# Kernel optimization log

Hardware: AMD Instinct MI355X
Metric: run time of the kernel (lower is better)

The kernel has to match this reference:

```python
import jax, jax.numpy as jnp
from jax import lax
import numpy as np

IMG = 448          # input image H=W
FEAT = 14          # attention map H=W
STR = IMG // FEAT  # 32: feature->image stride
OUT = 112          # crop resize target
RATIOS = [(4, 4), (3, 5), (5, 3), (6, 6), (5, 7), (7, 5)]
GROUPS = [(0, 3), (3, 6)]   # ratio groups for per-group NMS
N_LIST = [4, 3]
IOU_THRESHS = [0.25, 0.25]
PROPOSALN = 7
CLASSES = 200


def _build_coords():
    coords = []
    for (rh, rw) in RATIOS:
        for r in range(FEAT - rh + 1):
            for c in range(FEAT - rw + 1):
                coords.append([r * STR, c * STR, (r + rh) * STR - 1, (c + rw) * STR - 1])
    return np.array(coords, dtype=np.float32)

COORDS = jnp.asarray(_build_coords())                      # [602, 4] image-space boxes (inclusive)
WINDOW_NUMS = [(FEAT - rh + 1) * (FEAT - rw + 1) for rh, rw in RATIOS]
GROUP_BOUNDS = []
for (s, e) in GROUPS:
    GROUP_BOUNDS.append((sum(WINDOW_NUMS[:s]), sum(WINDOW_NUMS[:e])))


def _window_scores(att):
    # att: [B,1,FEAT,FEAT] -> [B, total_windows]; AvgPool2d(ratio, stride=1) per ratio, flattened row-major
    scs = []
    for (rh, rw) in RATIOS:
        s = lax.reduce_window(att[:, 0], 0.0, lax.add, (1, rh, rw), (1, 1, 1), 'VALID') / (rh * rw)
        scs.append(s.reshape(att.shape[0], -1))
    return jnp.concatenate(scs, axis=1)


def _iou(box, boxes):
    x0 = jnp.maximum(box[0], boxes[:, 0]); y0 = jnp.maximum(box[1], boxes[:, 1])
    x1 = jnp.minimum(box[2], boxes[:, 2]); y1 = jnp.minimum(box[3], boxes[:, 3])
    inter = jnp.maximum(x1 - x0 + 1, 0.0) * jnp.maximum(y1 - y0 + 1, 0.0)
    a1 = (box[2] - box[0] + 1) * (box[3] - box[1] + 1)
    a2 = (boxes[:, 2] - boxes[:, 0] + 1) * (boxes[:, 3] - boxes[:, 1] + 1)
    return inter / (a1 + a2 - inter)


def _nms(scores, boxes, n, thresh):
    # greedy NMS: pick argmax, suppress IoU>thresh, repeat n times
    def step(sc, _):
        idx = jnp.argmax(sc)
        iou = _iou(boxes[idx], boxes)
        sc = jnp.where(iou > thresh, -jnp.inf, sc).at[idx].set(-jnp.inf)
        return sc, idx
    _, idxs = lax.scan(step, scores, None, length=n)
    return idxs.astype(jnp.int32)


def _appm(att):
    all_scores = _window_scores(att)                        # [B, W]
    sg = lax.stop_gradient(all_scores)
    idx_parts = []
    for gi, (gs, ge) in enumerate(GROUP_BOUNDS):
        bx = COORDS[gs:ge]
        f = lambda s: _nms(s, bx, N_LIST[gi], IOU_THRESHS[gi])
        idx_parts.append(jax.vmap(f)(sg[:, gs:ge]) + gs)
    indices = jnp.concatenate(idx_parts, axis=1)            # [B, PROPOSALN]
    win_scores = jnp.take_along_axis(all_scores, indices, axis=1)
    return indices, win_scores, all_scores


_T = jnp.linspace(0.0, 1.0, OUT)


def _crop_resize(img, box):
    # bilinear crop+resize with align_corners=True semantics; img [3,H,W], box [4]
    rs = box[0] + (box[2] - box[0]) * _T
    cs = box[1] + (box[3] - box[1]) * _T
    r0f = jnp.floor(rs); c0f = jnp.floor(cs)
    wr = (rs - r0f)[None, :, None]
    wc = (cs - c0f)[None, None, :]
    r0 = r0f.astype(jnp.int32); c0 = c0f.astype(jnp.int32)
    r1 = jnp.minimum(r0 + 1, IMG - 1); c1 = jnp.minimum(c0 + 1, IMG - 1)
    g = lambda ri, ci: img[:, ri[:, None], ci[None, :]]
    top = (1 - wc) * g(r0, c0) + wc * g(r0, c1)
    bot = (1 - wc) * g(r1, c0) + wc * g(r1, c1)
    return (1 - wr) * top + wr * bot                        # [3, OUT, OUT]


def _encoder(x, ws, bs):
    h = x
    for w, b in zip(ws, bs):
        h = lax.conv_general_dilated(h, w, (2, 2), 'SAME', dimension_numbers=('NCHW', 'OIHW', 'NCHW'))
        h = jax.nn.relu(h + b[None, :, None, None])
    return h


def _head(feat, head_w, head_b):
    return jnp.mean(feat, axis=(2, 3)) @ head_w + head_b


def reference(x, att, w0, b0, w1, b1, w2, b2, w3, b3, w4, b4, head_w, head_b):
    ws = [w0, w1, w2, w3, w4]; bs = [b0, b1, b2, b3, b4]
    B = x.shape[0]
    labels = _head(_encoder(x, ws, bs), head_w, head_b)     # [B, CLASSES]
    indices, win_scores, all_scores = _appm(att)
    boxes = COORDS[indices]                                  # [B, PROPOSALN, 4]
    crop = lambda im, bxs: jax.vmap(lambda b: _crop_resize(im, b))(bxs)
    window_imgs = jax.vmap(crop)(x, boxes)                   # [B, P, 3, OUT, OUT]
    window_imgs = lax.stop_gradient(window_imgs).reshape(B * PROPOSALN, 3, OUT, OUT)  # .detach()
    win_logits = _head(_encoder(window_imgs, ws, bs), head_w, head_b)  # [B*P, CLASSES]
    coordinates = boxes.astype(jnp.int32)
    return labels, win_scores, win_logits, indices, all_scores, coordinates


def setup_inputs() -> dict:
    key = jax.random.key(0)
    ks = jax.random.split(key, 16)
    B = 16
    s = 0.05
    return {
        'x': jax.random.normal(ks[0], (B, 3, IMG, IMG), jnp.float32),
        'att': jax.random.uniform(ks[1], (B, 1, FEAT, FEAT), jnp.float32),
        'w0': jax.random.normal(ks[2], (64, 3, 3, 3), jnp.float32) * s,
        'b0': jax.random.normal(ks[3], (64,), jnp.float32) * s,
        'w1': jax.random.normal(ks[4], (128, 64, 3, 3), jnp.float32) * s,
        'b1': jax.random.normal(ks[5], (128,), jnp.float32) * s,
        'w2': jax.random.normal(ks[6], (256, 128, 3, 3), jnp.float32) * s,
        'b2': jax.random.normal(ks[7], (256,), jnp.float32) * s,
        'w3': jax.random.normal(ks[8], (512, 256, 3, 3), jnp.float32) * s,
        'b3': jax.random.normal(ks[9], (512,), jnp.float32) * s,
        'w4': jax.random.normal(ks[10], (512, 512, 3, 3), jnp.float32) * s,
        'b4': jax.random.normal(ks[11], (512,), jnp.float32) * s,
        'head_w': jax.random.normal(ks[12], (512, CLASSES), jnp.float32) * s,
        'head_b': jax.random.normal(ks[13], (CLASSES,), jnp.float32) * s,
    }
```

## Files before the change

kernel.cpp:

```cpp
#include <hip/hip_runtime.h>
#include <hip/hip_bf16.h>
#include <math.h>


#define OFF_LAB 0
#define OFF_WSC 3200
#define OFF_LOG 3312
#define OFF_IDX 25712
#define OFF_ALL 25824
#define OFF_CRD 35456

#define BS 256

typedef __attribute__((ext_vector_type(8))) short short8;
typedef __attribute__((ext_vector_type(4))) float f32x4;

static inline int cdiv(int a, int b) { return (a + b - 1) / b; }

__device__ __forceinline__ void win_decode(int w, int& rh, int& rw, int& r, int& c) {
  const int RH[6] = {4, 3, 5, 6, 5, 7};
  const int RW[6] = {4, 5, 3, 6, 7, 5};
  int rem = w;
#pragma unroll
  for (int i = 0; i < 6; ++i) {
    int nc = 15 - RW[i];
    int cnt = (15 - RH[i]) * nc;
    if (rem < cnt) { rh = RH[i]; rw = RW[i]; r = rem / nc; c = rem - (rem / nc) * nc; return; }
    rem -= cnt;
  }
  rh = 4; rw = 4; r = 0; c = 0;
}

__device__ __forceinline__ void win_to_box(int w, float* bb) {
  int rh, rw, r, c;
  win_decode(w, rh, rw, r, c);
  bb[0] = r * 32.f;
  bb[1] = c * 32.f;
  bb[2] = (r + rh) * 32.f - 1.f;
  bb[3] = (c + rw) * 32.f - 1.f;
}

__global__ void winscores_kernel(const float* __restrict__ att, float* __restrict__ s_all,
                                 float* __restrict__ out) {
  int idx = blockIdx.x * blockDim.x + threadIdx.x;
  if (idx >= 16 * 602) return;
  int b = idx / 602, w = idx - b * 602;
  int rh, rw, r, c;
  win_decode(w, rh, rw, r, c);
  const float* a = att + b * 196;
  float s = 0.f;
  for (int dr = 0; dr < rh; ++dr)
    for (int dc = 0; dc < rw; ++dc)
      s += a[(r + dr) * 14 + (c + dc)];
  float v = s / (float)(rh * rw);
  s_all[idx] = v;
  out[OFF_ALL + idx] = v;
}

__global__ void nms_kernel(const float* __restrict__ s_all, int* __restrict__ idx_i) {
  const int b = blockIdx.x, g = blockIdx.y;
  const int gs = g ? 361 : 0;
  const int cnt = g ? 241 : 361;
  const int nsel = g ? 3 : 4;
  const int obase = b * 7 + (g ? 4 : 0);
  __shared__ float sc[361];
  __shared__ float bx0[361], bx1[361], bx2[361], bx3[361];
  const int tid = threadIdx.x;
  for (int k = tid; k < cnt; k += 64) {
    sc[k] = s_all[b * 602 + gs + k];
    float bb[4];
    win_to_box(gs + k, bb);
    bx0[k] = bb[0]; bx1[k] = bb[1]; bx2[k] = bb[2]; bx3[k] = bb[3];
  }
  __syncthreads();
  for (int it = 0; it < nsel; ++it) {
    float bv = -INFINITY;
    int bi = 0x7fffffff;
    for (int k = tid; k < cnt; k += 64) {
      float v = sc[k];
      if (v > bv || (v == bv && k < bi)) { bv = v; bi = k; }
    }
#pragma unroll
    for (int off = 32; off > 0; off >>= 1) {
      float ov = __shfl_down(bv, off);
      int oi = __shfl_down(bi, off);
      if (ov > bv || (ov == bv && oi < bi)) { bv = ov; bi = oi; }
    }
    bi = __shfl(bi, 0);
    if (tid == 0) idx_i[obase + it] = gs + bi;
    float X0 = bx0[bi], X1 = bx1[bi], X2 = bx2[bi], X3 = bx3[bi];
    float a1 = (X2 - X0 + 1.f) * (X3 - X1 + 1.f);
    __syncthreads();
    for (int k = tid; k < cnt; k += 64) {
      float x0 = fmaxf(X0, bx0[k]);
      float y0 = fmaxf(X1, bx1[k]);
      float x1 = fminf(X2, bx2[k]);
      float y1 = fminf(X3, bx3[k]);
      float inter = fmaxf(x1 - x0 + 1.f, 0.f) * fmaxf(y1 - y0 + 1.f, 0.f);
      float a2 = (bx2[k] - bx0[k] + 1.f) * (bx3[k] - bx1[k] + 1.f);
      float iou = inter / (a1 + a2 - inter);
      if (iou > 0.25f) sc[k] = -INFINITY;
    }
    if (tid == 0) sc[bi] = -INFINITY;
    __syncthreads();
  }
}

__global__ void gather_kernel(const int* __restrict__ idx_i, const float* __restrict__ s_all,
                              float* __restrict__ boxes, float* __restrict__ out) {
  int t = blockIdx.x * blockDim.x + threadIdx.x;
  if (t >= 112) return;
  int b = t / 7;
  int w = idx_i[t];
  out[OFF_IDX + t] = (float)w;
  out[OFF_WSC + t] = s_all[b * 602 + w];
  float bb[4];
  win_to_box(w, bb);
#pragma unroll
  for (int k = 0; k < 4; ++k) {
    boxes[t * 4 + k] = bb[k];
    out[OFF_CRD + t * 4 + k] = bb[k];
  }
}

__global__ void crop_resize_kernel(const float* __restrict__ x, const float* __restrict__ boxes,
                                   float* __restrict__ wimgs) {
  int idx = blockIdx.x * blockDim.x + threadIdx.x;
  const int total = 112 * 3 * 112 * 112;
  if (idx >= total) return;
  int j = idx % 112;
  int i = (idx / 112) % 112;
  int ch = (idx / (112 * 112)) % 3;
  int bp = idx / (3 * 112 * 112);
  int b = bp / 7;
  const float* bx = boxes + bp * 4;
  float t_i = (float)i / 111.0f;
  float t_j = (float)j / 111.0f;
  float rs = bx[0] + (bx[2] - bx[0]) * t_i;
  float cs = bx[1] + (bx[3] - bx[1]) * t_j;
  float r0f = floorf(rs), c0f = floorf(cs);
  float wr = rs - r0f, wc = cs - c0f;
  int r0 = (int)r0f, c0 = (int)c0f;
  int r1 = min(r0 + 1, 447), c1 = min(c0 + 1, 447);
  const float* img = x + ((size_t)b * 3 + ch) * 448 * 448;
  float v00 = img[r0 * 448 + c0], v01 = img[r0 * 448 + c1];
  float v10 = img[r1 * 448 + c0], v11 = img[r1 * 448 + c1];
  float top = (1.f - wc) * v00 + wc * v01;
  float bot = (1.f - wc) * v10 + wc * v11;
  wimgs[idx] = (1.f - wr) * top + wr * bot;
}

__global__ void zf8_kernel(uint4* __restrict__ p, int n16) {
  int idx = blockIdx.x * blockDim.x + threadIdx.x;
  if (idx < n16) p[idx] = make_uint4(0, 0, 0, 0);
}

__global__ void packw_kernel(const float* __restrict__ w, __hip_bfloat16* __restrict__ dst,
                             int Cout, int Cin) {
  int idx = blockIdx.x * blockDim.x + threadIdx.x;
  int total = Cout * Cin * 9;
  if (idx >= total) return;
  int ci = idx % Cin;
  int rc = idx / Cin;
  int co = rc % Cout;
  int t = rc / Cout;
  dst[idx] = __float2bfloat16(w[((size_t)co * Cin + ci) * 9 + t]);
}

__global__ void packw0_kernel(const float* __restrict__ w, __hip_bfloat16* __restrict__ dst) {
  int idx = blockIdx.x * blockDim.x + threadIdx.x;
  if (idx >= 64 * 32) return;
  int co = idx >> 5, k = idx & 31;
  float v = 0.f;
  if (k < 27) {
    int t = k / 3, c = k - t * 3;
    v = w[((size_t)co * 3 + c) * 9 + t];
  }
  dst[idx] = __float2bfloat16(v);
}

__global__ void im2col3_kernel(const float* __restrict__ x, __hip_bfloat16* __restrict__ A,
                               int N, int Hin, int Hout) {
  int m = blockIdx.x * blockDim.x + threadIdx.x;
  int total = N * Hout * Hout;
  if (m >= total) return;
  int n = m / (Hout * Hout);
  int rem = m - n * (Hout * Hout);
  int oh = rem / Hout, ow = rem - (rem / Hout) * Hout;
  const float* xb = x + (size_t)n * 3 * Hin * Hin;
  __hip_bfloat16* a = A + (size_t)m * 32;
#pragma unroll
  for (int kh = 0; kh < 3; ++kh) {
#pragma unroll
    for (int kw = 0; kw < 3; ++kw) {
      int ih = 2 * oh + kh, iw = 2 * ow + kw;
      bool ok = (ih < Hin) && (iw < Hin);
#pragma unroll
      for (int c = 0; c < 3; ++c) {
        float v = ok ? xb[(size_t)c * Hin * Hin + (size_t)ih * Hin + iw] : 0.f;
        a[(kh * 3 + kw) * 3 + c] = __float2bfloat16(v);
      }
    }
  }
#pragma unroll
  for (int k = 27; k < 32; ++k) a[k] = __float2bfloat16(0.f);
}

template <bool IM2COL>
__global__ __launch_bounds__(256) void conv_mfma_kernel(
    const __hip_bfloat16* __restrict__ in, const __hip_bfloat16* __restrict__ wpk,
    const float* __restrict__ bias, __hip_bfloat16* __restrict__ outp,
    int M, int Hout, int Wout, int Hp, int Wp, int Cin, int Cout, int pad,
    int Hop, int Wop) {
  const int l = threadIdx.x & 63;
  const int w = threadIdx.x >> 6;
  const int px0 = blockIdx.y * 128 + w * 32;
  if (px0 >= M) return;
  const int co0 = blockIdx.x * 64;
  const int half = l >> 4;
  const int lr = l & 15;
  const int HWo = Hout * Wout;

  int mA0 = px0 + lr;      if (mA0 >= M) mA0 = M - 1;
  int mA1 = px0 + 16 + lr; if (mA1 >= M) mA1 = M - 1;
  const __hip_bfloat16* pA0;
  const __hip_bfloat16* pA1;
  if (IM2COL) {
    pA0 = in + (size_t)mA0 * 32 + half * 8;
    pA1 = in + (size_t)mA1 * 32 + half * 8;
  } else {
    int n0 = mA0 / HWo, r0 = mA0 - n0 * HWo, oh0 = r0 / Wout, ow0 = r0 - (r0 / Wout) * Wout;
    int n1 = mA1 / HWo, r1 = mA1 - n1 * HWo, oh1 = r1 / Wout, ow1 = r1 - (r1 / Wout) * Wout;
    pA0 = in + (((size_t)n0 * Hp + (2 * oh0 - pad + 1)) * Wp + (2 * ow0 - pad + 1)) * Cin +
          half * 8;
    pA1 = in + (((size_t)n1 * Hp + (2 * oh1 - pad + 1)) * Wp + (2 * ow1 - pad + 1)) * Cin +
          half * 8;
  }
  const __hip_bfloat16* pB = wpk + (size_t)(co0 + lr) * Cin + half * 8;
  const size_t sCo = (size_t)Cout * Cin;

  f32x4 acc[2][4];
#pragma unroll
  for (int ms = 0; ms < 2; ++ms)
#pragma unroll
    for (int s = 0; s < 4; ++s) acc[ms][s] = (f32x4){0.f, 0.f, 0.f, 0.f};

  const int nq = Cin >> 5;
  for (int q = 0; q < nq; ++q) {
    const int q32 = q << 5;
    if (IM2COL) {
      short8 a0 = *(const short8*)(pA0);
      short8 a1 = *(const short8*)(pA1);
#pragma unroll
      for (int s = 0; s < 4; ++s) {
        short8 b = *(const short8*)(pB + (size_t)s * 16 * Cin);
        acc[0][s] = __builtin_amdgcn_mfma_f32_16x16x32_bf16(a0, b, acc[0][s], 0, 0, 0);
        acc[1][s] = __builtin_amdgcn_mfma_f32_16x16x32_bf16(a1, b, acc[1][s], 0, 0, 0);
      }
    } else {
#pragma unroll
      for (int kh = 0; kh < 3; ++kh) {
#pragma unroll
        for (int kw = 0; kw < 3; ++kw) {
          const int dA = (kh * Wp + kw) * Cin + q32;
          short8 a0 = *(const short8*)(pA0 + dA);
          short8 a1 = *(const short8*)(pA1 + dA);
          const __hip_bfloat16* qb = pB + (size_t)(kh * 3 + kw) * sCo + q32;
#pragma unroll
          for (int s = 0; s < 4; ++s) {
            short8 b = *(const short8*)(qb + (size_t)s * 16 * Cin);
            acc[0][s] = __builtin_amdgcn_mfma_f32_16x16x32_bf16(a0, b, acc[0][s], 0, 0, 0);
            acc[1][s] = __builtin_amdgcn_mfma_f32_16x16x32_bf16(a1, b, acc[1][s], 0, 0, 0);
          }
        }
      }
    }
  }

  float bj0 = bias[co0 + lr];
  float bj1 = bias[co0 + 16 + lr];
  float bj2 = bias[co0 + 32 + lr];
  float bj3 = bias[co0 + 48 + lr];
#pragma unroll
  for (int ms = 0; ms < 2; ++ms) {
#pragma unroll
    for (int r = 0; r < 4; ++r) {
      int m = px0 + ms * 16 + half * 4 + r;
      if (m >= M) continue;
      int n = m / HWo, rem = m - n * HWo;
      int oh = rem / Wout, ow = rem - (rem / Wout) * Wout;
      __hip_bfloat16* ob =
          outp + (((size_t)n * Hop + oh + 1) * Wop + (ow + 1)) * Cout + co0 + lr;
      float v0 = fmaxf(acc[ms][0][r] + bj0, 0.f);
      float v1 = fmaxf(acc[ms][1][r] + bj1, 0.f);
      float v2 = fmaxf(acc[ms][2][r] + bj2, 0.f);
      float v3 = fmaxf(acc[ms][3][r] + bj3, 0.f);
      ob[0] = __float2bfloat16(v0);
      ob[16] = __float2bfloat16(v1);
      ob[32] = __float2bfloat16(v2);
      ob[48] = __float2bfloat16(v3);
    }
  }
}

__global__ void avgpool_nhwc_kernel(const __hip_bfloat16* __restrict__ feat,
                                    float* __restrict__ pooled, int Nimg, int H, int Hp, int C) {
  int idx = blockIdx.x * blockDim.x + threadIdx.x;
  if (idx >= Nimg * C) return;
  int n = idx / C, c = idx - n * C;
  float s = 0.f;
  for (int h = 1; h <= H; ++h)
    for (int ww = 1; ww <= H; ++ww)
      s += __bfloat162float(feat[(((size_t)n * Hp + h) * Hp + ww) * C + c]);
  pooled[idx] = s / (float)(H * H);
}

__global__ void head_kernel(const float* __restrict__ pooled, const float* __restrict__ hw,
                            const float* __restrict__ hb, float* __restrict__ outp, int M) {
  int idx = blockIdx.x * blockDim.x + threadIdx.x;
  if (idx >= M * 200) return;
  int m = idx / 200, c = idx - m * 200;
  float acc = hb[c];
  const float* pm = pooled + m * 512;
  for (int k = 0; k < 512; ++k) acc = fmaf(pm[k], hw[k * 200 + c], acc);
  outp[idx] = acc;
}

static void launch_conv(bool im2col, const __hip_bfloat16* in, const __hip_bfloat16* wpk,
                        const float* bv, __hip_bfloat16* dst, int M, int Hout, int Hp, int Cin,
                        int Cout, int pad, int Hop, hipStream_t s) {
  dim3 grid(Cout / 64, cdiv(M, 128));
  if (im2col)
    conv_mfma_kernel<true><<<grid, 256, 0, s>>>(in, wpk, bv, dst, M, Hout, Hout, Hp, Hp, Cin,
                                                Cout, pad, Hop, Hop);
  else
    conv_mfma_kernel<false><<<grid, 256, 0, s>>>(in, wpk, bv, dst, M, Hout, Hout, Hp, Hp, Cin,
                                                 Cout, pad, Hop, Hop);
}

static void zf(__hip_bfloat16* p, size_t n, hipStream_t s) {
  zf8_kernel<<<cdiv((int)(n / 8), BS), BS, 0, s>>>((uint4*)p, (int)(n / 8));
}

extern "C" void kernel_launch(void* const* d_in, const int* in_sizes, int n_in,
                              void* d_out, int out_size, void* d_ws, size_t ws_size,
                              hipStream_t stream) {
  const float* x = (const float*)d_in[0];
  const float* att = (const float*)d_in[1];
  const float* W[5] = {(const float*)d_in[2], (const float*)d_in[4], (const float*)d_in[6],
                       (const float*)d_in[8], (const float*)d_in[10]};
  const float* Bv[5] = {(const float*)d_in[3], (const float*)d_in[5], (const float*)d_in[7],
                        (const float*)d_in[9], (const float*)d_in[11]};
  const float* head_w = (const float*)d_in[12];
  const float* head_b = (const float*)d_in[13];
  float* out = (float*)d_out;
  float* ws = (float*)d_ws;

  size_t o = 0;
  float* s_all = ws + o;  o += 16 * 602;
  int* idx_i = (int*)(ws + o); o += 112;
  float* boxes = ws + o;  o += 112 * 4;
  float* pooled = ws + o; o += (size_t)112 * 512;
  float* wimgs = ws + o;  o += (size_t)112 * 3 * 112 * 112;
  __hip_bfloat16* hb = (__hip_bfloat16*)(ws + o);
  size_t h = 0;
  __hip_bfloat16* wpk0 = hb + h; h += 64 * 32;
  __hip_bfloat16* wpk1 = hb + h; h += (size_t)9 * 128 * 64;
  __hip_bfloat16* wpk2 = hb + h; h += (size_t)9 * 256 * 128;
  __hip_bfloat16* wpk3 = hb + h; h += (size_t)9 * 512 * 256;
  __hip_bfloat16* wpk4 = hb + h; h += (size_t)9 * 512 * 512;
  __hip_bfloat16* A_L0 = hb + h; h += (size_t)200704 * 32;
  __hip_bfloat16* bufA = hb + h; h += (size_t)4 * 226 * 226 * 64;
  __hip_bfloat16* bufB = hb + h; h += (size_t)4 * 114 * 114 * 128;
  __hip_bfloat16* bufC = hb + h; h += (size_t)56 * 16 * 16 * 256;
  __hip_bfloat16* fL3b = hb + h; h += (size_t)16 * 30 * 30 * 512;
  __hip_bfloat16* fL3c = hb + h; h += (size_t)112 * 9 * 9 * 512;
  __hip_bfloat16* featB = hb + h; h += (size_t)16 * 16 * 16 * 512;
  __hip_bfloat16* featC = hb + h; h += (size_t)112 * 6 * 6 * 512;

  winscores_kernel<<<cdiv(16 * 602, BS), BS, 0, stream>>>(att, s_all, out);
  nms_kernel<<<dim3(16, 2), 64, 0, stream>>>(s_all, idx_i);
  gather_kernel<<<1, 128, 0, stream>>>(idx_i, s_all, boxes, out);
  crop_resize_kernel<<<cdiv(112 * 3 * 112 * 112, BS), BS, 0, stream>>>(x, boxes, wimgs);

  packw0_kernel<<<cdiv(64 * 32, BS), BS, 0, stream>>>(W[0], wpk0);
  packw_kernel<<<cdiv(9 * 128 * 64, BS), BS, 0, stream>>>(W[1], wpk1, 128, 64);
  packw_kernel<<<cdiv(9 * 256 * 128, BS), BS, 0, stream>>>(W[2], wpk2, 256, 128);
  packw_kernel<<<cdiv(9 * 512 * 256, BS), BS, 0, stream>>>(W[3], wpk3, 512, 256);
  packw_kernel<<<cdiv(9 * 512 * 512, BS), BS, 0, stream>>>(W[4], wpk4, 512, 512);

  zf(bufA, (size_t)4 * 226 * 226 * 64, stream);
  zf(bufB, (size_t)4 * 114 * 114 * 128, stream);
  zf(bufC, (size_t)56 * 16 * 16 * 256, stream);
  zf(fL3b, (size_t)16 * 30 * 30 * 512, stream);
  zf(featB, (size_t)16 * 16 * 16 * 512, stream);
  for (int chunk = 0; chunk < 4; ++chunk) {
    int n0 = chunk * 4;
    im2col3_kernel<<<cdiv(200704, BS), BS, 0, stream>>>(x + (size_t)n0 * 3 * 448 * 448, A_L0, 4,
                                                        448, 224);
    launch_conv(true, A_L0, wpk0, Bv[0], bufA, 200704, 224, 0, 32, 64, 0, 226, stream);
    launch_conv(false, bufA, wpk1, Bv[1], bufB, 50176, 112, 226, 64, 128, 0, 114, stream);
    launch_conv(false, bufB, wpk2, Bv[2], bufC, 12544, 56, 114, 128, 256, 0, 58, stream);
    launch_conv(false, bufC, wpk3, Bv[3], fL3b + (size_t)n0 * 30 * 30 * 512, 3136, 28, 58, 256,
                512, 0, 30, stream);
  }
  launch_conv(false, fL3b, wpk4, Bv[4], featB, 16 * 196, 14, 30, 512, 512, 0, 16, stream);
  avgpool_nhwc_kernel<<<cdiv(16 * 512, BS), BS, 0, stream>>>(featB, pooled, 16, 14, 16, 512);
  head_kernel<<<cdiv(16 * 200, BS), BS, 0, stream>>>(pooled, head_w, head_b, out + OFF_LAB, 16);

  zf(bufA, (size_t)4 * 226 * 226 * 64, stream);
  zf(bufB, (size_t)4 * 114 * 114 * 128, stream);
  zf(bufC, (size_t)56 * 16 * 16 * 256, stream);
  zf(fL3c, (size_t)112 * 9 * 9 * 512, stream);
  zf(featC, (size_t)112 * 6 * 6 * 512, stream);
  for (int chunk = 0; chunk < 2; ++chunk) {
    int c0 = chunk * 56;
    im2col3_kernel<<<cdiv(175616, BS), BS, 0, stream>>>(wimgs + (size_t)c0 * 3 * 112 * 112, A_L0,
                                                        56, 112, 56);
    launch_conv(true, A_L0, wpk0, Bv[0], bufA, 175616, 56, 0, 32, 64, 0, 58, stream);
    launch_conv(false, bufA, wpk1, Bv[1], bufB, 43904, 28, 58, 64, 128, 0, 30, stream);
    launch_conv(false, bufB, wpk2, Bv[2], bufC, 10976, 14, 30, 128, 256, 0, 16, stream);
    launch_conv(false, bufC, wpk3, Bv[3], fL3c + (size_t)c0 * 9 * 9 * 512, 2744, 7, 16, 256, 512,
                0, 9, stream);
  }
  launch_conv(false, fL3c, wpk4, Bv[4], featC, 112 * 16, 4, 9, 512, 512, 1, 6, stream);
  avgpool_nhwc_kernel<<<cdiv(112 * 512, BS), BS, 0, stream>>>(featC, pooled, 112, 4, 6, 512);
  head_kernel<<<cdiv(112 * 200, BS), BS, 0, stream>>>(pooled, head_w, head_b, out + OFF_LOG, 112);
}
```

Before: 1.787 ms.

## Add split-K for deep conv layers and batch layer-3 across chunks

Adds a split-K path to the MFMA conv kernel: the grid gets a z dimension, each z slice accumulates a subset of input-channel blocks into an fp32 partial buffer, and a new reduce kernel sums the partials, adds bias, applies ReLU and writes bf16 NHWC output. Layer 3 now runs once over all images instead of once per chunk, because the layer-2 output buffer is enlarged to hold every chunk. Split-K is used for the small-M layer-4 convs (and for layer 3 on the crops) to fill more compute units. This trades extra fp32 partial traffic and an extra launch for more parallelism, and reuses the bufA and A_L0 regions as the partial buffer and as fL3c.

```diff
diff --git a/kernel.cpp b/kernel.cpp
--- a/kernel.cpp
+++ b/kernel.cpp
@@ -210,6 +210,7 @@
 __global__ __launch_bounds__(256) void conv_mfma_kernel(
     const __hip_bfloat16* __restrict__ in, const __hip_bfloat16* __restrict__ wpk,
     const float* __restrict__ bias, __hip_bfloat16* __restrict__ outp,
+    float* __restrict__ pbuf,
     int M, int Hout, int Wout, int Hp, int Wp, int Cin, int Cout, int pad,
     int Hop, int Wop) {
   const int l = threadIdx.x & 63;
@@ -246,7 +247,10 @@
     for (int s = 0; s < 4; ++s) acc[ms][s] = (f32x4){0.f, 0.f, 0.f, 0.f};
 
   const int nq = Cin >> 5;
-  for (int q = 0; q < nq; ++q) {
+  const int nqz = nq / gridDim.z;
+  const int qlo = blockIdx.z * nqz;
+  const int qhi = qlo + nqz;
+  for (int q = qlo; q < qhi; ++q) {
     const int q32 = q << 5;
     if (IM2COL) {
       short8 a0 = *(const short8*)(pA0);
@@ -277,30 +281,58 @@
     }
   }
 
-  float bj0 = bias[co0 + lr];
-  float bj1 = bias[co0 + 16 + lr];
-  float bj2 = bias[co0 + 32 + lr];
-  float bj3 = bias[co0 + 48 + lr];
-#pragma unroll
-  for (int ms = 0; ms < 2; ++ms) {
-#pragma unroll
-    for (int r = 0; r < 4; ++r) {
-      int m = px0 + ms * 16 + half * 4 + r;
-      if (m >= M) continue;
-      int n = m / HWo, rem = m - n * HWo;
-      int oh = rem / Wout, ow = rem - (rem / Wout) * Wout;
-      __hip_bfloat16* ob =
-          outp + (((size_t)n * Hop + oh + 1) * Wop + (ow + 1)) * Cout + co0 + lr;
-      float v0 = fmaxf(acc[ms][0][r] + bj0, 0.f);
-      float v1 = fmaxf(acc[ms][1][r] + bj1, 0.f);
-      float v2 = fmaxf(acc[ms][2][r] + bj2, 0.f);
-      float v3 = fmaxf(acc[ms][3][r] + bj3, 0.f);
-      ob[0] = __float2bfloat16(v0);
-      ob[16] = __float2bfloat16(v1);
-      ob[32] = __float2bfloat16(v2);
-      ob[48] = __float2bfloat16(v3);
-    }
-  }
+  if (gridDim.z == 1) {
+    float bj0 = bias[co0 + lr];
+    float bj1 = bias[co0 + 16 + lr];
+    float bj2 = bias[co0 + 32 + lr];
+    float bj3 = bias[co0 + 48 + lr];
+#pragma unroll
+    for (int ms = 0; ms < 2; ++ms) {
+#pragma unroll
+      for (int r = 0; r < 4; ++r) {
+        int m = px0 + ms * 16 + half * 4 + r;
+        if (m >= M) continue;
+        int n = m / HWo, rem = m - n * HWo;
+        int oh = rem / Wout, ow = rem - (rem / Wout) * Wout;
+        __hip_bfloat16* ob =
+            outp + (((size_t)n * Hop + oh + 1) * Wop + (ow + 1)) * Cout + co0 + lr;
+        ob[0] = __float2bfloat16(fmaxf(acc[ms][0][r] + bj0, 0.f));
+        ob[16] = __float2bfloat16(fmaxf(acc[ms][1][r] + bj1, 0.f));
+        ob[32] = __float2bfloat16(fmaxf(acc[ms][2][r] + bj2, 0.f));
+        ob[48] = __float2bfloat16(fmaxf(acc[ms][3][r] + bj3, 0.f));
+      }
+    }
+  } else {
+    float* pz = pbuf + (size_t)blockIdx.z * M * Cout;
+#pragma unroll
+    for (int ms = 0; ms < 2; ++ms) {
+#pragma unroll
+      for (int r = 0; r < 4; ++r) {
+        int m = px0 + ms * 16 + half * 4 + r;
+        if (m >= M) continue;
+        float* pm = pz + (size_t)m * Cout + co0 + lr;
+        pm[0] = acc[ms][0][r];
+        pm[16] = acc[ms][1][r];
+        pm[32] = acc[ms][2][r];
+        pm[48] = acc[ms][3][r];
+      }
+    }
+  }
+}
+
+__global__ void reduce_nhwc_kernel(const float* __restrict__ pbuf, const float* __restrict__ bias,
+                                   __hip_bfloat16* __restrict__ outp, int M, int Cout, int nz,
+                                   int Hout, int Wout, int Hop, int Wop) {
+  int idx = blockIdx.x * blockDim.x + threadIdx.x;
+  if (idx >= M * Cout) return;
+  int m = idx / Cout, co = idx - m * Cout;
+  float s = 0.f;
+  for (int z = 0; z < nz; ++z) s += pbuf[(size_t)z * M * Cout + idx];
+  s = fmaxf(s + bias[co], 0.f);
+  int HWo = Hout * Wout;
+  int n = m / HWo, rem = m - n * HWo;
+  int oh = rem / Wout, ow = rem - (rem / Wout) * Wout;
+  outp[(((size_t)n * Hop + oh + 1) * Wop + (ow + 1)) * Cout + co] = __float2bfloat16(s);
 }
 
 __global__ void avgpool_nhwc_kernel(const __hip_bfloat16* __restrict__ feat,
@@ -327,15 +359,18 @@
 }
 
 static void launch_conv(bool im2col, const __hip_bfloat16* in, const __hip_bfloat16* wpk,
-                        const float* bv, __hip_bfloat16* dst, int M, int Hout, int Hp, int Cin,
-                        int Cout, int pad, int Hop, hipStream_t s) {
-  dim3 grid(Cout / 64, cdiv(M, 128));
+                        const float* bv, __hip_bfloat16* dst, float* pbuf, int nz, int M,
+                        int Hout, int Hp, int Cin, int Cout, int pad, int Hop, hipStream_t s) {
+  dim3 grid(Cout / 64, cdiv(M, 128), nz);
   if (im2col)
-    conv_mfma_kernel<true><<<grid, 256, 0, s>>>(in, wpk, bv, dst, M, Hout, Hout, Hp, Hp, Cin,
-                                                Cout, pad, Hop, Hop);
+    conv_mfma_kernel<true><<<grid, 256, 0, s>>>(in, wpk, bv, dst, pbuf, M, Hout, Hout, Hp, Hp,
+                                                Cin, Cout, pad, Hop, Hop);
   else
-    conv_mfma_kernel<false><<<grid, 256, 0, s>>>(in, wpk, bv, dst, M, Hout, Hout, Hp, Hp, Cin,
-                                                 Cout, pad, Hop, Hop);
+    conv_mfma_kernel<false><<<grid, 256, 0, s>>>(in, wpk, bv, dst, pbuf, M, Hout, Hout, Hp, Hp,
+                                                 Cin, Cout, pad, Hop, Hop);
+  if (nz > 1)
+    reduce_nhwc_kernel<<<cdiv(M * Cout, BS), BS, 0, s>>>(pbuf, bv, dst, M, Cout, nz, Hout, Hout,
+                                                         Hop, Hop);
 }
 
 static void zf(__hip_bfloat16* p, size_t n, hipStream_t s) {
@@ -370,11 +405,12 @@
   __hip_bfloat16* wpk3 = hb + h; h += (size_t)9 * 512 * 256;
   __hip_bfloat16* wpk4 = hb + h; h += (size_t)9 * 512 * 512;
   __hip_bfloat16* A_L0 = hb + h; h += (size_t)200704 * 32;
+  __hip_bfloat16* fL3c = A_L0;
   __hip_bfloat16* bufA = hb + h; h += (size_t)4 * 226 * 226 * 64;
+  float* pK = (float*)bufA;
   __hip_bfloat16* bufB = hb + h; h += (size_t)4 * 114 * 114 * 128;
-  __hip_bfloat16* bufC = hb + h; h += (size_t)56 * 16 * 16 * 256;
+  __hip_bfloat16* bufC16 = hb + h; h += (size_t)16 * 58 * 58 * 256;
   __hip_bfloat16* fL3b = hb + h; h += (size_t)16 * 30 * 30 * 512;
-  __hip_bfloat16* fL3c = hb + h; h += (size_t)112 * 9 * 9 * 512;
   __hip_bfloat16* featB = hb + h; h += (size_t)16 * 16 * 16 * 512;
   __hip_bfloat16* featC = hb + h; h += (size_t)112 * 6 * 6 * 512;
 
@@ -391,39 +427,44 @@
 
   zf(bufA, (size_t)4 * 226 * 226 * 64, stream);
   zf(bufB, (size_t)4 * 114 * 114 * 128, stream);
-  zf(bufC, (size_t)56 * 16 * 16 * 256, stream);
+  zf(bufC16, (size_t)16 * 58 * 58 * 256, stream);
   zf(fL3b, (size_t)16 * 30 * 30 * 512, stream);
   zf(featB, (size_t)16 * 16 * 16 * 512, stream);
   for (int chunk = 0; chunk < 4; ++chunk) {
     int n0 = chunk * 4;
     im2col3_kernel<<<cdiv(200704, BS), BS, 0, stream>>>(x + (size_t)n0 * 3 * 448 * 448, A_L0, 4,
                                                         448, 224);
-    launch_conv(true, A_L0, wpk0, Bv[0], bufA, 200704, 224, 0, 32, 64, 0, 226, stream);
-    launch_conv(false, bufA, wpk1, Bv[1], bufB, 50176, 112, 226, 64, 128, 0, 114, stream);
-    launch_conv(false, bufB, wpk2, Bv[2], bufC, 12544, 56, 114, 128, 256, 0, 58, stream);
-    launch_conv(false, bufC, wpk3, Bv[3], fL3b + (size_t)n0 * 30 * 30 * 512, 3136, 28, 58, 256,
-                512, 0, 30, stream);
-  }
-  launch_conv(false, fL3b, wpk4, Bv[4], featB, 16 * 196, 14, 30, 512, 512, 0, 16, stream);
+    launch_conv(true, A_L0, wpk0, Bv[0], bufA, nullptr, 1, 200704, 224, 0, 32, 64, 0, 226,
+                stream);
+    launch_conv(false, bufA, wpk1, Bv[1], bufB, nullptr, 1, 50176, 112, 226, 64, 128, 0, 114,
+                stream);
+    launch_conv(false, bufB, wpk2, Bv[2], bufC16 + (size_t)n0 * 58 * 58 * 256, nullptr, 1, 12544,
+                56, 114, 128, 256, 0, 58, stream);
+  }
+  launch_conv(false, bufC16, wpk3, Bv[3], fL3b, nullptr, 1, 50176, 28, 58, 256, 512, 0, 30,
+              stream);
+  launch_conv(false, fL3b, wpk4, Bv[4], featB, pK, 4, 3136, 14, 30, 512, 512, 0, 16, stream);
   avgpool_nhwc_kernel<<<cdiv(16 * 512, BS), BS, 0, stream>>>(featB, pooled, 16, 14, 16, 512);
   head_kernel<<<cdiv(16 * 200, BS), BS, 0, stream>>>(pooled, head_w, head_b, out + OFF_LAB, 16);
 
   zf(bufA, (size_t)4 * 226 * 226 * 64, stream);
   zf(bufB, (size_t)4 * 114 * 114 * 128, stream);
-  zf(bufC, (size_t)56 * 16 * 16 * 256, stream);
-  zf(fL3c, (size_t)112 * 9 * 9 * 512, stream);
+  zf(bufC16, (size_t)16 * 58 * 58 * 256, stream);
   zf(featC, (size_t)112 * 6 * 6 * 512, stream);
   for (int chunk = 0; chunk < 2; ++chunk) {
     int c0 = chunk * 56;
     im2col3_kernel<<<cdiv(175616, BS), BS, 0, stream>>>(wimgs + (size_t)c0 * 3 * 112 * 112, A_L0,
                                                         56, 112, 56);
-    launch_conv(true, A_L0, wpk0, Bv[0], bufA, 175616, 56, 0, 32, 64, 0, 58, stream);
-    launch_conv(false, bufA, wpk1, Bv[1], bufB, 43904, 28, 58, 64, 128, 0, 30, stream);
-    launch_conv(false, bufB, wpk2, Bv[2], bufC, 10976, 14, 30, 128, 256, 0, 16, stream);
-    launch_conv(false, bufC, wpk3, Bv[3], fL3c + (size_t)c0 * 9 * 9 * 512, 2744, 7, 16, 256, 512,
-                0, 9, stream);
-  }
-  launch_conv(false, fL3c, wpk4, Bv[4], featC, 112 * 16, 4, 9, 512, 512, 1, 6, stream);
+    launch_conv(true, A_L0, wpk0, Bv[0], bufA + (size_t)0, nullptr, 1, 175616, 56, 0, 32, 64, 0,
+                58, stream);
+    launch_conv(false, bufA, wpk1, Bv[1], bufB, nullptr, 1, 43904, 28, 58, 64, 128, 0, 30,
+                stream);
+    launch_conv(false, bufB, wpk2, Bv[2], bufC16 + (size_t)c0 * 16 * 16 * 256, nullptr, 1, 10976,
+                14, 30, 128, 256, 0, 16, stream);
+  }
+  zf(fL3c, (size_t)112 * 9 * 9 * 512, stream);
+  launch_conv(false, bufC16, wpk3, Bv[3], fL3c, pK, 2, 5488, 7, 16, 256, 512, 0, 9, stream);
+  launch_conv(false, fL3c, wpk4, Bv[4], featC, pK, 4, 1792, 4, 9, 512, 512, 1, 6, stream);
   avgpool_nhwc_kernel<<<cdiv(112 * 512, BS), BS, 0, stream>>>(featC, pooled, 112, 4, 6, 512);
   head_kernel<<<cdiv(112 * 200, BS), BS, 0, stream>>>(pooled, head_w, head_b, out + OFF_LOG, 112);
 }
```

Measured after the change: 2.074 ms. 16.0% more time.
